# Optimization experiments

Hardware: AMD Instinct MI355X
Metric: run time of the kernel (lower is better)

## Reference

```python
import jax, jax.numpy as jnp
import numpy as np

N_NODES = 100000
N_EDGES = 600000
D_IN = 128
D_OUT = 128

def gcn_conv(x, src, dst, W, b, n):
    # PyG GCNConv: h = X W; out_i = sum_j norm_ij * h_j + b, with self-loops and
    # symmetric normalization norm_ij = deg_i^{-1/2} deg_j^{-1/2}.
    deg = jax.ops.segment_sum(jnp.ones_like(dst, dtype=x.dtype), dst, num_segments=n)
    dinv = jnp.where(deg > 0, jax.lax.rsqrt(deg), 0.0)
    norm = dinv[src] * dinv[dst]            # [E]
    h = x @ W                                # [N, D_out]
    msg = h[src] * norm[:, None]             # gather + scale, [E, D_out]
    out = jax.ops.segment_sum(msg, dst, num_segments=n)
    return out + b

def setup_inputs() -> dict:
    key = jax.random.key(0)
    ks = jax.random.split(key, 8)
    x = jax.random.normal(ks[0], (N_NODES, D_IN), dtype=jnp.float32)
    edge_index = jax.random.randint(ks[1], (2, N_EDGES), 0, N_NODES, dtype=jnp.int64)
    s = (1.0 / np.sqrt(D_IN)).astype(np.float32) if isinstance(np.sqrt(D_IN), np.ndarray) else np.float32(1.0 / np.sqrt(D_IN))
    W1 = jax.random.normal(ks[2], (D_IN, D_OUT), dtype=jnp.float32) * s
    b1 = jnp.zeros((D_OUT,), dtype=jnp.float32)
    W2 = jax.random.normal(ks[3], (D_OUT, D_OUT), dtype=jnp.float32) * np.float32(1.0 / np.sqrt(D_OUT))
    b2 = jnp.zeros((D_OUT,), dtype=jnp.float32)
    Wfc = jax.random.normal(ks[4], (D_IN, D_OUT), dtype=jnp.float32) * s
    bfc = jnp.zeros((D_OUT,), dtype=jnp.float32)
    return {"x": x, "edge_index": edge_index, "W1": W1, "b1": b1,
            "W2": W2, "b2": b2, "Wfc": Wfc, "bfc": bfc}

def reference(x, edge_index, W1, b1, W2, b2, Wfc, bfc):
    n = x.shape[0]
    loop = jnp.arange(n, dtype=edge_index.dtype)
    src = jnp.concatenate([edge_index[0], loop])  # add self-loops
    dst = jnp.concatenate([edge_index[1], loop])
    res = x @ Wfc + bfc                           # linear residual branch
    h = jax.nn.relu(gcn_conv(x, src, dst, W1, b1, n))
    h = jax.nn.relu(gcn_conv(h, src, dst, W2, b2, n))
    return h + res
```

## Files before the change

### kernel.cpp

```cpp
#include <hip/hip_runtime.h>
#include <hip/hip_bf16.h>

#define D 128

typedef __bf16 bf16x8 __attribute__((ext_vector_type(8)));
typedef float f32x16 __attribute__((ext_vector_type(16)));

union U16 { uint4 u; bf16x8 v; };

static __device__ __forceinline__ unsigned short f2bf(float f) {
    unsigned u = __float_as_uint(f);
    unsigned r = (u + 0x7fffu + ((u >> 16) & 1u)) >> 16;
    return (unsigned short)r;
}
static __device__ __forceinline__ float bf2f(unsigned short s) {
    return __uint_as_float(((unsigned)s) << 16);
}
static __device__ __forceinline__ float u2f_lo(unsigned x) { return __uint_as_float(x << 16); }
static __device__ __forceinline__ float u2f_hi(unsigned x) { return __uint_as_float(x & 0xffff0000u); }

__global__ __launch_bounds__(256) void k_prep(
        const float* __restrict__ W1, const float* __restrict__ W2, const float* __restrict__ Wf,
        unsigned short* __restrict__ W1h, unsigned short* __restrict__ W1l,
        unsigned short* __restrict__ W2h, unsigned short* __restrict__ W2l,
        unsigned short* __restrict__ Wfh, unsigned short* __restrict__ Wfl,
        int* __restrict__ cnt, int n) {
    int idx = blockIdx.x * 256 + threadIdx.x;
    if (idx < 3 * 16384) {
        int which = idx >> 14;
        int local = idx & 16383;
        int k = local >> 7, c = local & 127;
        const float* W = (which == 0) ? W1 : (which == 1) ? W2 : Wf;
        unsigned short* Wh = (which == 0) ? W1h : (which == 1) ? W2h : Wfh;
        unsigned short* Wl = (which == 0) ? W1l : (which == 1) ? W2l : Wfl;
        float v = W[k * 128 + c];
        unsigned short h = f2bf(v);
        unsigned short l = f2bf(v - bf2f(h));
        Wh[c * 128 + k] = h;
        Wl[c * 128 + k] = l;
    }
    if (idx < n) cnt[idx] = 0;
}


__global__ __launch_bounds__(256) void k_hist(const int* __restrict__ dst,
                                              int* __restrict__ cnt, int e) {
    int i = blockIdx.x * 256 + threadIdx.x;
    if (i < e) atomicAdd(&cnt[dst[i]], 1);
}

#define SCAN_CHUNK 1024

__global__ __launch_bounds__(256) void k_scan_local(const int* __restrict__ cnt,
                                                    int* __restrict__ ptr,
                                                    int* __restrict__ sums, int n) {
    __shared__ int tsum[256];
    const int t = threadIdx.x;
    const int base = blockIdx.x * SCAN_CHUNK + t * 4;
    int v[4]; int s = 0;
    #pragma unroll
    for (int i = 0; i < 4; ++i) {
        int idx = base + i;
        v[i] = (idx < n) ? cnt[idx] : 0;
        s += v[i];
    }
    tsum[t] = s;
    __syncthreads();
    for (int off = 1; off < 256; off <<= 1) {
        int x = (t >= off) ? tsum[t - off] : 0;
        __syncthreads();
        tsum[t] += x;
        __syncthreads();
    }
    int run = (t > 0) ? tsum[t - 1] : 0;
    if (t == 255) sums[blockIdx.x] = tsum[255];
    #pragma unroll
    for (int i = 0; i < 4; ++i) {
        int idx = base + i;
        if (idx < n) ptr[idx] = run;
        run += v[i];
    }
}

__global__ __launch_bounds__(256) void k_scan_sums(int* __restrict__ sums, int nChunks) {
    __shared__ int ls[256];
    const int t = threadIdx.x;
    ls[t] = (t < nChunks) ? sums[t] : 0;
    __syncthreads();
    for (int off = 1; off < 256; off <<= 1) {
        int x = (t >= off) ? ls[t - off] : 0;
        __syncthreads();
        ls[t] += x;
        __syncthreads();
    }
    if (t < nChunks) sums[t] = (t > 0) ? ls[t - 1] : 0;
}

__global__ __launch_bounds__(256) void k_scan_add(int* __restrict__ ptr,
                                                  const int* __restrict__ sums,
                                                  int* __restrict__ cnt,
                                                  float* __restrict__ dinv,
                                                  int n, int e) {
    int i = blockIdx.x * 256 + threadIdx.x;
    if (i < n) {
        ptr[i] += sums[i >> 10];
        dinv[i] = rsqrtf((float)(1 + cnt[i]));
        cnt[i] = 0;
    }
    if (i == 0) ptr[n] = e;
}

__global__ __launch_bounds__(256) void k_fill(const int* __restrict__ src,
                                              const int* __restrict__ dst,
                                              const int* __restrict__ ptr,
                                              int* __restrict__ fill,
                                              const float* __restrict__ dinv,
                                              uint2* __restrict__ csr, int e) {
    int i = blockIdx.x * 256 + threadIdx.x;
    if (i < e) {
        int d = dst[i];
        int s = src[i];
        int slot = ptr[d] + atomicAdd(&fill[d], 1);
        csr[slot] = make_uint2((unsigned)s, __float_as_uint(dinv[s]));
    }
}

#define APAD 136

__global__ __launch_bounds__(256, 2) void k_gemm_dual(
        const float* __restrict__ A,
        const unsigned short* __restrict__ B1h, const unsigned short* __restrict__ B1l,
        const unsigned short* __restrict__ B2h, const unsigned short* __restrict__ B2l,
        const float* __restrict__ bias2,
        unsigned short* __restrict__ out1,
        float* __restrict__ out2,
        int M, int nTiles) {
    __shared__ __align__(16) unsigned short As[2][32][APAD];

    const int tid = threadIdx.x;
    const int wave = tid >> 6;
    const int lane = tid & 63;
    const int l31 = lane & 31;
    const int quad8 = (lane >> 5) * 8;
    const int col = wave * 32 + l31;

    U16 b1h[8], b1l[8], b2h[8], b2l[8];
    #pragma unroll
    for (int ks = 0; ks < 8; ++ks) {
        const size_t bo = (size_t)col * D + ks * 16 + quad8;
        b1h[ks].u = *(const uint4*)(B1h + bo);
        b1l[ks].u = *(const uint4*)(B1l + bo);
        b2h[ks].u = *(const uint4*)(B2h + bo);
        b2l[ks].u = *(const uint4*)(B2l + bo);
    }
    const float bv = bias2[col];

    for (int t = blockIdx.x; t < nTiles; t += gridDim.x) {
        const int row0 = t * 32;

        #pragma unroll
        for (int i = 0; i < 4; ++i) {
            int f = tid + i * 256;
            int r = f >> 5, c4 = (f & 31) * 4;
            int rg = row0 + r; if (rg >= M) rg = M - 1;
            float4 v = *(const float4*)(A + (size_t)rg * D + c4);
            ushort4 hq, lq;
            hq.x = f2bf(v.x); hq.y = f2bf(v.y); hq.z = f2bf(v.z); hq.w = f2bf(v.w);
            lq.x = f2bf(v.x - bf2f(hq.x)); lq.y = f2bf(v.y - bf2f(hq.y));
            lq.z = f2bf(v.z - bf2f(hq.z)); lq.w = f2bf(v.w - bf2f(hq.w));
            *(ushort4*)&As[0][r][c4] = hq;
            *(ushort4*)&As[1][r][c4] = lq;
        }
        __syncthreads();

        f32x16 acc1, acc2;
        #pragma unroll
        for (int r = 0; r < 16; ++r) { acc1[r] = 0.f; acc2[r] = 0.f; }

        #pragma unroll
        for (int ks = 0; ks < 8; ++ks) {
            U16 ah, al;
            ah.u = *(const uint4*)&As[0][l31][ks * 16 + quad8];
            al.u = *(const uint4*)&As[1][l31][ks * 16 + quad8];
            acc1 = __builtin_amdgcn_mfma_f32_32x32x16_bf16(ah.v, b1h[ks].v, acc1, 0, 0, 0);
            acc2 = __builtin_amdgcn_mfma_f32_32x32x16_bf16(ah.v, b2h[ks].v, acc2, 0, 0, 0);
            acc1 = __builtin_amdgcn_mfma_f32_32x32x16_bf16(ah.v, b1l[ks].v, acc1, 0, 0, 0);
            acc2 = __builtin_amdgcn_mfma_f32_32x32x16_bf16(ah.v, b2l[ks].v, acc2, 0, 0, 0);
            acc1 = __builtin_amdgcn_mfma_f32_32x32x16_bf16(al.v, b1h[ks].v, acc1, 0, 0, 0);
            acc2 = __builtin_amdgcn_mfma_f32_32x32x16_bf16(al.v, b2h[ks].v, acc2, 0, 0, 0);
        }
        __syncthreads();

        #pragma unroll
        for (int reg = 0; reg < 16; ++reg) {
            const int r = (reg & 3) + 8 * (reg >> 2) + 4 * (lane >> 5);
            const int rg = row0 + r;
            if (rg < M) {
                out1[(size_t)rg * D + col] = f2bf(acc1[reg]);
                out2[(size_t)rg * D + col] = acc2[reg] + bv;
            }
        }
    }
}

__global__ __launch_bounds__(256, 4) void k_gemm_rr_bf(
        const unsigned short* __restrict__ A,
        const unsigned short* __restrict__ Bh, const unsigned short* __restrict__ Bl,
        unsigned short* __restrict__ outb,
        int M, int nTiles) {
    __shared__ __align__(16) unsigned short As[32][APAD];

    const int tid = threadIdx.x;
    const int wave = tid >> 6;
    const int lane = tid & 63;
    const int l31 = lane & 31;
    const int quad8 = (lane >> 5) * 8;
    const int col = wave * 32 + l31;

    U16 bh[8], bl[8];
    #pragma unroll
    for (int ks = 0; ks < 8; ++ks) {
        const size_t bo = (size_t)col * D + ks * 16 + quad8;
        bh[ks].u = *(const uint4*)(Bh + bo);
        bl[ks].u = *(const uint4*)(Bl + bo);
    }

    for (int t = blockIdx.x; t < nTiles; t += gridDim.x) {
        const int row0 = t * 32;

        #pragma unroll
        for (int i = 0; i < 2; ++i) {
            int f = tid + i * 256;
            int r = f >> 4, c8 = (f & 15) * 8;
            int rg = row0 + r; if (rg >= M) rg = M - 1;
            *(uint4*)&As[r][c8] = *(const uint4*)(A + (size_t)rg * D + c8);
        }
        __syncthreads();

        f32x16 acc;
        #pragma unroll
        for (int r = 0; r < 16; ++r) acc[r] = 0.f;

        #pragma unroll
        for (int ks = 0; ks < 8; ++ks) {
            U16 ah;
            ah.u = *(const uint4*)&As[l31][ks * 16 + quad8];
            acc = __builtin_amdgcn_mfma_f32_32x32x16_bf16(ah.v, bh[ks].v, acc, 0, 0, 0);
            acc = __builtin_amdgcn_mfma_f32_32x32x16_bf16(ah.v, bl[ks].v, acc, 0, 0, 0);
        }
        __syncthreads();

        #pragma unroll
        for (int reg = 0; reg < 16; ++reg) {
            const int r = (reg & 3) + 8 * (reg >> 2) + 4 * (lane >> 5);
            const int rg = row0 + r;
            if (rg < M) outb[(size_t)rg * D + col] = f2bf(acc[reg]);
        }
    }
}

__global__ __launch_bounds__(256) void k_gather_w(const int* __restrict__ ptr,
                                                  const uint2* __restrict__ csr,
                                                  const float* __restrict__ dinv,
                                                  const unsigned short* __restrict__ h,
                                                  const float* __restrict__ bias,
                                                  const float* __restrict__ res,
                                                  float* __restrict__ outf,
                                                  unsigned short* __restrict__ outb,
                                                  int N) {
    const int g = threadIdx.x >> 5;
    const int lane = threadIdx.x & 31;
    const int i = blockIdx.x * 8 + g;
    if (i >= N) return;

    const int p0 = ptr[i];
    const int p1 = ptr[i + 1];
    const float di = dinv[i];

    float a0 = 0.f, a1 = 0.f, a2 = 0.f, a3 = 0.f;
    const unsigned* cb = (const unsigned*)csr;
    int j = p0;
    for (; j + 4 <= p1; j += 4) {
        const uint4 e0 = *(const uint4*)(cb + 2 * (size_t)j);
        const uint4 e1 = *(const uint4*)(cb + 2 * (size_t)j + 4);
        const float c0 = __uint_as_float(e0.y);
        const float c1 = __uint_as_float(e0.w);
        const float c2 = __uint_as_float(e1.y);
        const float c3 = __uint_as_float(e1.w);
        const uint2 u0 = *(const uint2*)(h + (size_t)e0.x * D + lane * 4);
        const uint2 u1 = *(const uint2*)(h + (size_t)e0.z * D + lane * 4);
        const uint2 u2 = *(const uint2*)(h + (size_t)e1.x * D + lane * 4);
        const uint2 u3 = *(const uint2*)(h + (size_t)e1.z * D + lane * 4);
        a0 = fmaf(c0, u2f_lo(u0.x), a0); a1 = fmaf(c0, u2f_hi(u0.x), a1);
        a2 = fmaf(c0, u2f_lo(u0.y), a2); a3 = fmaf(c0, u2f_hi(u0.y), a3);
        a0 = fmaf(c1, u2f_lo(u1.x), a0); a1 = fmaf(c1, u2f_hi(u1.x), a1);
        a2 = fmaf(c1, u2f_lo(u1.y), a2); a3 = fmaf(c1, u2f_hi(u1.y), a3);
        a0 = fmaf(c2, u2f_lo(u2.x), a0); a1 = fmaf(c2, u2f_hi(u2.x), a1);
        a2 = fmaf(c2, u2f_lo(u2.y), a2); a3 = fmaf(c2, u2f_hi(u2.y), a3);
        a0 = fmaf(c3, u2f_lo(u3.x), a0); a1 = fmaf(c3, u2f_hi(u3.x), a1);
        a2 = fmaf(c3, u2f_lo(u3.y), a2); a3 = fmaf(c3, u2f_hi(u3.y), a3);
    }
    for (; j < p1; ++j) {
        const uint2 e = csr[j];
        const float c = __uint_as_float(e.y);
        const uint2 u = *(const uint2*)(h + (size_t)e.x * D + lane * 4);
        a0 = fmaf(c, u2f_lo(u.x), a0);
        a1 = fmaf(c, u2f_hi(u.x), a1);
        a2 = fmaf(c, u2f_lo(u.y), a2);
        a3 = fmaf(c, u2f_hi(u.y), a3);
    }

    const uint2 us = *(const uint2*)(h + (size_t)i * D + lane * 4);
    const float4 bv = *(const float4*)(bias + lane * 4);
    const float self = di * di;
    float o0 = fmaxf(di * a0 + self * u2f_lo(us.x) + bv.x, 0.0f);
    float o1 = fmaxf(di * a1 + self * u2f_hi(us.x) + bv.y, 0.0f);
    float o2 = fmaxf(di * a2 + self * u2f_lo(us.y) + bv.z, 0.0f);
    float o3 = fmaxf(di * a3 + self * u2f_hi(us.y) + bv.w, 0.0f);
    if (outb) {
        ushort4 q = {f2bf(o0), f2bf(o1), f2bf(o2), f2bf(o3)};
        *(ushort4*)(outb + (size_t)i * D + lane * 4) = q;
    } else {
        const float4 rv = *(const float4*)(res + (size_t)i * D + lane * 4);
        float4 o = {o0 + rv.x, o1 + rv.y, o2 + rv.z, o3 + rv.w};
        *(float4*)(outf + (size_t)i * D + lane * 4) = o;
    }
}


extern "C" void kernel_launch(void* const* d_in, const int* in_sizes, int n_in,
                              void* d_out, int out_size, void* d_ws, size_t ws_size,
                              hipStream_t stream) {
    const int N = in_sizes[0] / D;
    const int E = in_sizes[1] / 2;

    const float* x   = (const float*)d_in[0];
    const int*   ei  = (const int*)d_in[1];
    const int*   src = ei;
    const int*   dst = ei + E;
    const float* W1  = (const float*)d_in[2];
    const float* b1  = (const float*)d_in[3];
    const float* W2  = (const float*)d_in[4];
    const float* b2  = (const float*)d_in[5];
    const float* Wfc = (const float*)d_in[6];
    const float* bfc = (const float*)d_in[7];
    float* out = (float*)d_out;

    char* ws = (char*)d_ws;
    size_t off = 0;
    auto alloc = [&](size_t bytes) { char* p = ws + off; off += (bytes + 255) & ~(size_t)255; return p; };
    float* dinv    = (float*)alloc((size_t)N * 4);
    int*   cnt     = (int*)  alloc((size_t)N * 4);
    int*   ptr     = (int*)  alloc((size_t)(N + 1) * 4);
    int*   sums    = (int*)  alloc(256 * 4);
    uint2* csr     = (uint2*)alloc((size_t)(E + 64) * sizeof(uint2));
    unsigned short* W1h = (unsigned short*)alloc(128 * 128 * 2);
    unsigned short* W1l = (unsigned short*)alloc(128 * 128 * 2);
    unsigned short* W2h = (unsigned short*)alloc(128 * 128 * 2);
    unsigned short* W2l = (unsigned short*)alloc(128 * 128 * 2);
    unsigned short* Wfh = (unsigned short*)alloc(128 * 128 * 2);
    unsigned short* Wfl = (unsigned short*)alloc(128 * 128 * 2);
    unsigned short* h    = (unsigned short*)alloc((size_t)N * D * 2);
    unsigned short* hb16 = (unsigned short*)alloc((size_t)N * D * 2);

    const int nBlk    = (N + 255) / 256;
    const int eBlk    = (E + 255) / 256;
    const int aBlk    = (N + 7) / 8;
    const int nChunks = (N + SCAN_CHUNK - 1) / SCAN_CHUNK;
    const int nTiles  = (N + 31) / 32;
    const int gBlk    = nTiles < 1024 ? nTiles : 1024;
    const int pBlk    = (nBlk > 192) ? nBlk : 192;

    k_prep<<<pBlk, 256, 0, stream>>>(W1, W2, Wfc, W1h, W1l, W2h, W2l, Wfh, Wfl, cnt, N);

    k_hist<<<eBlk, 256, 0, stream>>>(dst, cnt, E);
    k_scan_local<<<nChunks, 256, 0, stream>>>(cnt, ptr, sums, N);
    k_scan_sums<<<1, 256, 0, stream>>>(sums, nChunks);
    k_scan_add<<<nBlk, 256, 0, stream>>>(ptr, sums, cnt, dinv, N, E);
    k_fill<<<eBlk, 256, 0, stream>>>(src, dst, ptr, cnt, dinv, csr, E);

    k_gemm_dual<<<gBlk, 256, 0, stream>>>(x, W1h, W1l, Wfh, Wfl, bfc, h, out, N, nTiles);

    k_gather_w<<<aBlk, 256, 0, stream>>>(ptr, csr, dinv, h, b1, nullptr, nullptr, hb16, N);

    k_gemm_rr_bf<<<gBlk, 256, 0, stream>>>(hb16, W2h, W2l, h, N, nTiles);

    k_gather_w<<<aBlk, 256, 0, stream>>>(ptr, csr, dinv, h, b2, out, out, nullptr, N);
}
```

Measured before the change: 294.6 us.

## Split dual GEMM across 512-thread blocks and unroll gather tail

The dual GEMM now launches 512 threads per block. Waves 0-3 compute the W1 product and waves 4-7 compute the residual Wfc product, so each wave holds half as many B fragments and runs a single accumulator chain. This lowers register pressure and raises occupancy, while the A tile staged in shared memory stays shared by both halves. Separately, the gather kernel's scalar remainder loop becomes a branch-free block of up to three masked loads, and the self and bias loads are hoisted earlier to overlap latency.

```diff
diff --git a/kernel.cpp b/kernel.cpp
--- a/kernel.cpp
+++ b/kernel.cpp
@@ -127,7 +127,7 @@
 
 #define APAD 136
 
-__global__ __launch_bounds__(256, 2) void k_gemm_dual(
+__global__ __launch_bounds__(512, 4) void k_gemm_dual(
         const float* __restrict__ A,
         const unsigned short* __restrict__ B1h, const unsigned short* __restrict__ B1l,
         const unsigned short* __restrict__ B2h, const unsigned short* __restrict__ B2l,
@@ -142,16 +142,18 @@
     const int lane = tid & 63;
     const int l31 = lane & 31;
     const int quad8 = (lane >> 5) * 8;
-    const int col = wave * 32 + l31;
-
-    U16 b1h[8], b1l[8], b2h[8], b2l[8];
+    const int col = (wave & 3) * 32 + l31;
+    const int sel = wave >> 2;
+
+    const unsigned short* __restrict__ Bh = sel ? B2h : B1h;
+    const unsigned short* __restrict__ Bl = sel ? B2l : B1l;
+
+    U16 bh[8], bl[8];
     #pragma unroll
     for (int ks = 0; ks < 8; ++ks) {
         const size_t bo = (size_t)col * D + ks * 16 + quad8;
-        b1h[ks].u = *(const uint4*)(B1h + bo);
-        b1l[ks].u = *(const uint4*)(B1l + bo);
-        b2h[ks].u = *(const uint4*)(B2h + bo);
-        b2l[ks].u = *(const uint4*)(B2l + bo);
+        bh[ks].u = *(const uint4*)(Bh + bo);
+        bl[ks].u = *(const uint4*)(Bl + bo);
     }
     const float bv = bias2[col];
 
@@ -159,8 +161,8 @@
         const int row0 = t * 32;
 
         #pragma unroll
-        for (int i = 0; i < 4; ++i) {
-            int f = tid + i * 256;
+        for (int i = 0; i < 2; ++i) {
+            int f = tid + i * 512;
             int r = f >> 5, c4 = (f & 31) * 4;
             int rg = row0 + r; if (rg >= M) rg = M - 1;
             float4 v = *(const float4*)(A + (size_t)rg * D + c4);
@@ -173,31 +175,34 @@
         }
         __syncthreads();
 
-        f32x16 acc1, acc2;
-        #pragma unroll
-        for (int r = 0; r < 16; ++r) { acc1[r] = 0.f; acc2[r] = 0.f; }
+        f32x16 acc;
+        #pragma unroll
+        for (int r = 0; r < 16; ++r) acc[r] = 0.f;
 
         #pragma unroll
         for (int ks = 0; ks < 8; ++ks) {
             U16 ah, al;
             ah.u = *(const uint4*)&As[0][l31][ks * 16 + quad8];
             al.u = *(const uint4*)&As[1][l31][ks * 16 + quad8];
-            acc1 = __builtin_amdgcn_mfma_f32_32x32x16_bf16(ah.v, b1h[ks].v, acc1, 0, 0, 0);
-            acc2 = __builtin_amdgcn_mfma_f32_32x32x16_bf16(ah.v, b2h[ks].v, acc2, 0, 0, 0);
-            acc1 = __builtin_amdgcn_mfma_f32_32x32x16_bf16(ah.v, b1l[ks].v, acc1, 0, 0, 0);
-            acc2 = __builtin_amdgcn_mfma_f32_32x32x16_bf16(ah.v, b2l[ks].v, acc2, 0, 0, 0);
-            acc1 = __builtin_amdgcn_mfma_f32_32x32x16_bf16(al.v, b1h[ks].v, acc1, 0, 0, 0);
-            acc2 = __builtin_amdgcn_mfma_f32_32x32x16_bf16(al.v, b2h[ks].v, acc2, 0, 0, 0);
-        }
-        __syncthreads();
-
-        #pragma unroll
-        for (int reg = 0; reg < 16; ++reg) {
-            const int r = (reg & 3) + 8 * (reg >> 2) + 4 * (lane >> 5);
-            const int rg = row0 + r;
-            if (rg < M) {
-                out1[(size_t)rg * D + col] = f2bf(acc1[reg]);
-                out2[(size_t)rg * D + col] = acc2[reg] + bv;
+            acc = __builtin_amdgcn_mfma_f32_32x32x16_bf16(ah.v, bh[ks].v, acc, 0, 0, 0);
+            acc = __builtin_amdgcn_mfma_f32_32x32x16_bf16(ah.v, bl[ks].v, acc, 0, 0, 0);
+            acc = __builtin_amdgcn_mfma_f32_32x32x16_bf16(al.v, bh[ks].v, acc, 0, 0, 0);
+        }
+        __syncthreads();
+
+        if (sel == 0) {
+            #pragma unroll
+            for (int reg = 0; reg < 16; ++reg) {
+                const int r = (reg & 3) + 8 * (reg >> 2) + 4 * (lane >> 5);
+                const int rg = row0 + r;
+                if (rg < M) out1[(size_t)rg * D + col] = f2bf(acc[reg]);
+            }
+        } else {
+            #pragma unroll
+            for (int reg = 0; reg < 16; ++reg) {
+                const int r = (reg & 3) + 8 * (reg >> 2) + 4 * (lane >> 5);
+                const int rg = row0 + r;
+                if (rg < M) out2[(size_t)rg * D + col] = acc[reg] + bv;
             }
         }
     }
@@ -276,6 +281,9 @@
     const int p0 = ptr[i];
     const int p1 = ptr[i + 1];
     const float di = dinv[i];
+
+    const uint2 us = *(const uint2*)(h + (size_t)i * D + lane * 4);
+    const float4 bvv = *(const float4*)(bias + lane * 4);
 
     float a0 = 0.f, a1 = 0.f, a2 = 0.f, a3 = 0.f;
     const unsigned* cb = (const unsigned*)csr;
@@ -300,23 +308,32 @@
         a0 = fmaf(c3, u2f_lo(u3.x), a0); a1 = fmaf(c3, u2f_hi(u3.x), a1);
         a2 = fmaf(c3, u2f_lo(u3.y), a2); a3 = fmaf(c3, u2f_hi(u3.y), a3);
     }
-    for (; j < p1; ++j) {
-        const uint2 e = csr[j];
-        const float c = __uint_as_float(e.y);
-        const uint2 u = *(const uint2*)(h + (size_t)e.x * D + lane * 4);
-        a0 = fmaf(c, u2f_lo(u.x), a0);
-        a1 = fmaf(c, u2f_hi(u.x), a1);
-        a2 = fmaf(c, u2f_lo(u.y), a2);
-        a3 = fmaf(c, u2f_hi(u.y), a3);
-    }
-
-    const uint2 us = *(const uint2*)(h + (size_t)i * D + lane * 4);
-    const float4 bv = *(const float4*)(bias + lane * 4);
+    const int r = p1 - j;
+    if (r > 0) {
+        const int j1 = (r > 1) ? j + 1 : j;
+        const int j2 = (r > 2) ? j + 2 : j;
+        const uint2 e0 = csr[j];
+        const uint2 e1 = csr[j1];
+        const uint2 e2 = csr[j2];
+        const float c0 = __uint_as_float(e0.y);
+        const float c1 = (r > 1) ? __uint_as_float(e1.y) : 0.f;
+        const float c2 = (r > 2) ? __uint_as_float(e2.y) : 0.f;
+        const uint2 u0 = *(const uint2*)(h + (size_t)e0.x * D + lane * 4);
+        const uint2 u1 = *(const uint2*)(h + (size_t)e1.x * D + lane * 4);
+        const uint2 u2 = *(const uint2*)(h + (size_t)e2.x * D + lane * 4);
+        a0 = fmaf(c0, u2f_lo(u0.x), a0); a1 = fmaf(c0, u2f_hi(u0.x), a1);
+        a2 = fmaf(c0, u2f_lo(u0.y), a2); a3 = fmaf(c0, u2f_hi(u0.y), a3);
+        a0 = fmaf(c1, u2f_lo(u1.x), a0); a1 = fmaf(c1, u2f_hi(u1.x), a1);
+        a2 = fmaf(c1, u2f_lo(u1.y), a2); a3 = fmaf(c1, u2f_hi(u1.y), a3);
+        a0 = fmaf(c2, u2f_lo(u2.x), a0); a1 = fmaf(c2, u2f_hi(u2.x), a1);
+        a2 = fmaf(c2, u2f_lo(u2.y), a2); a3 = fmaf(c2, u2f_hi(u2.y), a3);
+    }
+
     const float self = di * di;
-    float o0 = fmaxf(di * a0 + self * u2f_lo(us.x) + bv.x, 0.0f);
-    float o1 = fmaxf(di * a1 + self * u2f_hi(us.x) + bv.y, 0.0f);
-    float o2 = fmaxf(di * a2 + self * u2f_lo(us.y) + bv.z, 0.0f);
-    float o3 = fmaxf(di * a3 + self * u2f_hi(us.y) + bv.w, 0.0f);
+    float o0 = fmaxf(di * a0 + self * u2f_lo(us.x) + bvv.x, 0.0f);
+    float o1 = fmaxf(di * a1 + self * u2f_hi(us.x) + bvv.y, 0.0f);
+    float o2 = fmaxf(di * a2 + self * u2f_lo(us.y) + bvv.z, 0.0f);
+    float o3 = fmaxf(di * a3 + self * u2f_hi(us.y) + bvv.w, 0.0f);
     if (outb) {
         ushort4 q = {f2bf(o0), f2bf(o1), f2bf(o2), f2bf(o3)};
         *(ushort4*)(outb + (size_t)i * D + lane * 4) = q;
@@ -379,7 +396,7 @@
     k_scan_add<<<nBlk, 256, 0, stream>>>(ptr, sums, cnt, dinv, N, E);
     k_fill<<<eBlk, 256, 0, stream>>>(src, dst, ptr, cnt, dinv, csr, E);
 
-    k_gemm_dual<<<gBlk, 256, 0, stream>>>(x, W1h, W1l, Wfh, Wfl, bfc, h, out, N, nTiles);
+    k_gemm_dual<<<gBlk, 512, 0, stream>>>(x, W1h, W1l, Wfh, Wfl, bfc, h, out, N, nTiles);
 
     k_gather_w<<<aBlk, 256, 0, stream>>>(ptr, csr, dinv, h, b1, nullptr, nullptr, hb16, N);
 
```

Result: no change. 294.0 us (-0.2%).
